# Kernel tuning notes

Measured on AMD Instinct MI355X. Metric: run time of the kernel, lower is better.

Reference implementation:

```python
import jax, jax.numpy as jnp
import numpy as np

K = 256      # embedding size k
STATE = 128  # latent state size
IN = 64      # external input size
OBS = 64     # observation size
L = 512      # sequence length (time-major)
B = 256      # batch size


def _glorot(key, shape):
    return jax.random.normal(key, shape, dtype=jnp.float32) / float(np.sqrt(shape[0]))


def setup_inputs():
    key = jax.random.key(0)
    ks = jax.random.split(key, 12)
    p = {}
    p["external_input_seq"] = jax.random.normal(ks[0], (L, B, IN), dtype=jnp.float32)
    p["observations_seq"] = jax.random.normal(ks[1], (L, B, OBS), dtype=jnp.float32)
    p["eps"] = jax.random.normal(ks[2], (L, B, STATE), dtype=jnp.float32)  # reparam noise
    # PreProcess: Linear + tanh
    p["Wu"] = _glorot(ks[3], (IN, K)); p["bu"] = jnp.zeros((K,), jnp.float32)
    p["Wx"] = _glorot(ks[4], (OBS, K)); p["bx"] = jnp.zeros((K,), jnp.float32)
    # input_rnn: vanilla tanh RNN, 1 layer, k -> k
    p["W_ih"] = _glorot(ks[5], (K, K)); p["b_ih"] = jnp.zeros((K,), jnp.float32)
    p["W_hh"] = _glorot(ks[6], (K, K)); p["b_hh"] = jnp.zeros((K,), jnp.float32)
    # posterior_a_layer: MLP(2k, k, k, 1) = Linear -> tanh -> Linear
    p["Wa1"] = _glorot(ks[7], (2 * K, K)); p["ba1"] = jnp.zeros((K,), jnp.float32)
    p["Wa2"] = _glorot(ks[8], (K, K)); p["ba2"] = jnp.zeros((K,), jnp.float32)

    def dblock_params(k1, in_dim, hid, out):
        kk = jax.random.split(k1, 4)
        return (_glorot(kk[0], (in_dim, hid)), jnp.zeros((hid,), jnp.float32),
                _glorot(kk[1], (in_dim, hid)), jnp.zeros((hid,), jnp.float32),
                _glorot(kk[2], (hid, out)), jnp.zeros((out,), jnp.float32),
                _glorot(kk[3], (hid, out)), jnp.zeros((out,), jnp.float32))

    names = ["f1_W", "f1_b", "f2_W", "f2_b", "mu_W", "mu_b", "ls_W", "ls_b"]
    for pref, kk in (("post_", ks[9]), ("prior_", ks[10])):
        vals = dblock_params(kk, STATE + K, 2 * K, STATE)
        for n, v in zip(names, vals):
            p[pref + n] = v
    return p


def _dblock(x, f1_W, f1_b, f2_W, f2_b, mu_W, mu_b, ls_W, ls_b):
    # TD-VAE DBlock: gated hidden, then mu / logsigma heads
    t = jnp.tanh(x @ f1_W + f1_b) * jax.nn.sigmoid(x @ f2_W + f2_b)
    return t @ mu_W + mu_b, t @ ls_W + ls_b


def reference(external_input_seq, observations_seq, eps, Wu, bu, Wx, bx,
              W_ih, b_ih, W_hh, b_hh, Wa1, ba1, Wa2, ba2,
              post_f1_W, post_f1_b, post_f2_W, post_f2_b, post_mu_W, post_mu_b, post_ls_W, post_ls_b,
              prior_f1_W, prior_f1_b, prior_f2_W, prior_f2_b, prior_mu_W, prior_mu_b, prior_ls_W, prior_ls_b):
    batch = external_input_seq.shape[1]
    u_emb = jnp.tanh(external_input_seq @ Wu + bu)   # [L,B,K]
    x_emb = jnp.tanh(observations_seq @ Wx + bx)     # [L,B,K]

    # input_rnn (tanh RNN) over time, d0 = 0 (memory_state=None)
    def rnn_step(d, x):
        d_new = jnp.tanh(x @ W_ih + b_ih + d @ W_hh + b_hh)
        return d_new, d_new
    d0 = jnp.zeros((batch, W_hh.shape[0]), dtype=u_emb.dtype)
    dn, d_seq = jax.lax.scan(rnn_step, d0, u_emb)    # dn [B,K], d_seq [L,B,K]

    # posterior_a_layer: pointwise MLP; flip(0) then flip(0) is a no-op for a pointwise map
    ad = jnp.concatenate([d_seq, x_emb], axis=-1)    # [L,B,2K]
    a_seq = jnp.tanh(ad @ Wa1 + ba1) @ Wa2 + ba2     # [L,B,K]

    state_size = post_mu_W.shape[1]
    z0 = jnp.zeros((batch, state_size), dtype=u_emb.dtype)

    def step(z_prev, inp):
        a_t, d_t, e_t = inp
        mean_res, logsigma = _dblock(jnp.concatenate([z_prev, a_t], axis=-1),
                                     post_f1_W, post_f1_b, post_f2_W, post_f2_b,
                                     post_mu_W, post_mu_b, post_ls_W, post_ls_b)
        prior_mean = _dblock(jnp.concatenate([z_prev, d_t], axis=-1),
                             prior_f1_W, prior_f1_b, prior_f2_W, prior_f2_b,
                             prior_mu_W, prior_mu_b, prior_ls_W, prior_ls_b)[0]
        mu = prior_mean + mean_res
        # cov = diag(exp(logsigma)) -> std = exp(0.5*logsigma); reparameterized sample
        z_new = mu + jnp.exp(0.5 * logsigma) * e_t
        return z_new, (mu, logsigma)

    zn, (state_mu, state_logsigma) = jax.lax.scan(step, z0, (a_seq, d_seq, eps))
    return state_mu, state_logsigma, dn, zn
```

## Files before the change

### kernel.cpp

```cpp
#include <hip/hip_runtime.h>

#define LSEQ 512
#define BATCH 256
#define KDIM 256
#define STATE 128

using f32x4  = __attribute__((ext_vector_type(4))) float;
using short8 = __attribute__((ext_vector_type(8))) short;
using u32x2  = __attribute__((ext_vector_type(2))) unsigned int;
using u32x4  = __attribute__((ext_vector_type(4))) unsigned int;

__device__ __forceinline__ float bf2f(unsigned short u){
  return __uint_as_float(((unsigned int)u) << 16);
}
__device__ __forceinline__ unsigned short f2bf(float f){
  unsigned int u = __float_as_uint(f);
  u += 0x7FFFu + ((u >> 16) & 1u);
  return (unsigned short)(u >> 16);
}
__device__ __forceinline__ float fast_tanh(float x){
  float ax = fabsf(x);
  float e  = __expf(2.0f * ax);
  float t  = 1.0f - 2.0f / (e + 1.0f);
  return copysignf(t, x);
}
__device__ __forceinline__ float fast_sig(float x){
  return 1.0f / (1.0f + __expf(-x));
}
__device__ __forceinline__ f32x4 mfma16(short8 a, short8 b, f32x4 c){
  return __builtin_amdgcn_mfma_f32_16x16x32_bf16(a, b, c, 0, 0, 0);
}

__device__ __forceinline__ int swz128 (int b){ return b ^ ((((b >> 7) & 7) << 4)); }
__device__ __forceinline__ int swz256 (int b){ return b ^ ((((b >> 8) & 7) << 4)); }
__device__ __forceinline__ int swz512 (int b){ return b ^ ((((b >> 9) & 7) << 4)); }

__device__ __forceinline__ void st_b128_ic(void* p, u32x4 v){
  asm volatile("global_store_dwordx4 %0, %1, off sc0 sc1" :: "v"(p), "v"(v) : "memory");
}
__device__ __forceinline__ void st_b64_ic(void* p, u32x2 v){
  asm volatile("global_store_dwordx2 %0, %1, off sc0 sc1" :: "v"(p), "v"(v) : "memory");
}
#define LD2_IC(dst, p) asm volatile("global_load_dwordx2 %0, %1, off sc0 sc1" : "=v"(dst) : "v"(p) : "memory")

__device__ __forceinline__ f32x4 cvt4(u32x2 q){
  f32x4 r;
  r[0] = __uint_as_float(q[0] << 16);
  r[1] = __uint_as_float(q[0] & 0xFFFF0000u);
  r[2] = __uint_as_float(q[1] << 16);
  r[3] = __uint_as_float(q[1] & 0xFFFF0000u);
  return r;
}

struct WDesc { const float* src; unsigned short* dst; int K, N, ld, rowoff, coloff; };
struct WDescs { WDesc d[24]; };

__global__ __launch_bounds__(256,4) void convert_weights(WDescs ds){
  WDesc w = ds.d[blockIdx.y];
  int total = w.K * w.N;
  int idx = blockIdx.x * 256 + threadIdx.x;
  if (idx < total){
    int n = idx / w.K;
    int k = idx - n * w.K;
    w.dst[idx] = f2bf(w.src[(size_t)(w.rowoff + k) * w.ld + w.coloff + n]);
  }
}

__global__ __launch_bounds__(256,1) void init_flags(int* flags){
  flags[blockIdx.x * 256 + threadIdx.x] = 0;
}

__global__ __launch_bounds__(256,4) void compose_GA(
    const float* __restrict__ Wa2, const float* __restrict__ ba2,
    const unsigned short* __restrict__ fAp,
    const float* __restrict__ pf1b, const float* __restrict__ pf2b,
    unsigned short* __restrict__ GA, float* __restrict__ gb)
{
  const int n = blockIdx.x;
  const int k2 = threadIdx.x;
  const unsigned short* fr = fAp + (size_t)n * 256;
  const float* wr = Wa2 + (size_t)k2 * 256;
  float s = 0.f;
  for (int j = 0; j < 256; j++) s += wr[j] * bf2f(fr[j]);
  GA[(size_t)n * 256 + k2] = f2bf(s);
  if (k2 == 0){
    float b = 0.f;
    for (int j = 0; j < 256; j++) b += ba2[j] * bf2f(fr[j]);
    gb[n] = b + ((n < 512) ? pf1b[n] : pf2b[n - 512]);
  }
}

struct GArg {
  const void* A; const unsigned short* Bt; const float* bias; const float* bias2;
  unsigned short* C; int lda, ldc, coff, K, act, a_f32;
};
struct GArg2 {
  const unsigned short* A; const unsigned short* Bt; const float* bias; const float* bias2;
  unsigned short* C; int lda, ldc, coff, K, act;
};

__device__ void gemm_multi_body(const GArg ga, int bx, int by, int tid, char* lsraw){
  char* lsA = lsraw;
  char* lsB = lsraw + 16384;
  const int wave = tid >> 6, lane = tid & 63;
  const int col_l = lane & 15, rgrp = lane >> 4;
  const int m0 = bx * 128, n0 = by * 128;
  const int wm = (wave >> 1) * 64, wn = (wave & 1) * 64;

  f32x4 acc[4][4];
  const f32x4 z4 = {0.f,0.f,0.f,0.f};
  #pragma unroll
  for (int i=0;i<4;i++){ acc[i][0]=z4; acc[i][1]=z4; acc[i][2]=z4; acc[i][3]=z4; }

  const int srow = tid >> 1;
  const int sbe  = (tid & 1) * 32;

  for (int k0 = 0; k0 < ga.K; k0 += 64){
    uint4 av[4], bv[4];
    if (ga.a_f32){
      const float* Ap = (const float*)ga.A + (size_t)(m0 + srow) * ga.lda + k0 + sbe;
      uint4 fv[8];
      #pragma unroll
      for (int i=0;i<8;i++) fv[i] = *(const uint4*)((const char*)Ap + i*16);
      #pragma unroll
      for (int i=0;i<4;i++){
        const float* f = (const float*)&fv[i*2];
        uint4 o;
        o.x = (unsigned)f2bf(f[0]) | ((unsigned)f2bf(f[1]) << 16);
        o.y = (unsigned)f2bf(f[2]) | ((unsigned)f2bf(f[3]) << 16);
        o.z = (unsigned)f2bf(f[4]) | ((unsigned)f2bf(f[5]) << 16);
        o.w = (unsigned)f2bf(f[6]) | ((unsigned)f2bf(f[7]) << 16);
        av[i] = o;
      }
    } else {
      const unsigned short* Ap = (const unsigned short*)ga.A + (size_t)(m0 + srow) * ga.lda + k0 + sbe;
      #pragma unroll
      for (int i=0;i<4;i++) av[i] = *(const uint4*)((const char*)Ap + i*16);
    }
    const unsigned short* Bp = ga.Bt + (size_t)(n0 + srow) * ga.K + k0 + sbe;
    #pragma unroll
    for (int i=0;i<4;i++) bv[i] = *(const uint4*)((const char*)Bp + i*16);

    __syncthreads();
    #pragma unroll
    for (int i=0;i<4;i++){
      *(uint4*)(lsA + swz128(srow*128 + sbe*2 + i*16)) = av[i];
      *(uint4*)(lsB + swz128(srow*128 + sbe*2 + i*16)) = bv[i];
    }
    __syncthreads();
    #pragma unroll
    for (int kk=0; kk<2; kk++){
      short8 af[4], bfr[4];
      #pragma unroll
      for (int mt=0; mt<4; mt++)
        af[mt] = *(const short8*)(lsA + swz128((wm + mt*16 + col_l)*128 + kk*64 + rgrp*16));
      #pragma unroll
      for (int nt=0; nt<4; nt++)
        bfr[nt] = *(const short8*)(lsB + swz128((wn + nt*16 + col_l)*128 + kk*64 + rgrp*16));
      #pragma unroll
      for (int mt=0; mt<4; mt++)
        #pragma unroll
        for (int nt=0; nt<4; nt++)
          acc[mt][nt] = mfma16(af[mt], bfr[nt], acc[mt][nt]);
    }
  }
  #pragma unroll
  for (int nt=0; nt<4; nt++){
    int col = n0 + wn + nt*16 + col_l;
    const float* bsrc = (col < 512) ? ga.bias : ga.bias2;
    float bb = bsrc ? bsrc[col & 511] : 0.0f;
    #pragma unroll
    for (int mt=0; mt<4; mt++){
      #pragma unroll
      for (int r=0; r<4; r++){
        int row = m0 + wm + mt*16 + rgrp*4 + r;
        float v = acc[mt][nt][r] + bb;
        if (ga.act == 1) v = fast_tanh(v);
        ga.C[(size_t)row * ga.ldc + ga.coff + col] = f2bf(v);
      }
    }
  }
}

__device__ void gemm_glds_body(const GArg2 ga, int bx, int by, int tid, char* lsraw){
  const int wave = tid >> 6, lane = tid & 63;
  const int col_l = lane & 15, rgrp = lane >> 4;
  const int m0 = bx * 128, n0 = by * 128;
  const int wm = (wave >> 1) * 64, wn = (wave & 1) * 64;

  const int lrow = lane >> 3;
  const int scol = (((lane & 7) ^ lrow) << 3);

  auto STAGE = [&](int k0, int buf){
    #pragma unroll
    for (int c = 0; c < 4; c++){
      int srow = wave*32 + c*8 + lrow;
      const unsigned short* pa = ga.A  + (size_t)(m0 + srow) * ga.lda + k0 + scol;
      const unsigned short* pb = ga.Bt + (size_t)(n0 + srow) * ga.K  + k0 + scol;
      __builtin_amdgcn_global_load_lds(
          (const __attribute__((address_space(1))) unsigned int*)pa,
          (__attribute__((address_space(3))) unsigned int*)(lsraw + buf*32768 + wave*4096 + c*1024),
          16, 0, 0);
      __builtin_amdgcn_global_load_lds(
          (const __attribute__((address_space(1))) unsigned int*)pb,
          (__attribute__((address_space(3))) unsigned int*)(lsraw + buf*32768 + 16384 + wave*4096 + c*1024),
          16, 0, 0);
    }
  };

  f32x4 acc[4][4];
  const f32x4 z4 = {0.f,0.f,0.f,0.f};
  #pragma unroll
  for (int i=0;i<4;i++){ acc[i][0]=z4; acc[i][1]=z4; acc[i][2]=z4; acc[i][3]=z4; }

  const int niter = ga.K >> 6;
  STAGE(0, 0);

  for (int i = 0; i < niter; i++){
    if (i + 1 < niter){
      STAGE((i+1)*64, (i+1) & 1);
      asm volatile("s_waitcnt vmcnt(8)" ::: "memory");
    } else {
      asm volatile("s_waitcnt vmcnt(0)" ::: "memory");
    }
    __syncthreads();
    const char* la = lsraw + (i&1)*32768;
    const char* lb = la + 16384;
    #pragma unroll
    for (int kk=0; kk<2; kk++){
      short8 af[4], bfr[4];
      #pragma unroll
      for (int mt=0; mt<4; mt++)
        af[mt] = *(const short8*)(la + swz128((wm + mt*16 + col_l)*128 + kk*64 + rgrp*16));
      #pragma unroll
      for (int nt=0; nt<4; nt++)
        bfr[nt] = *(const short8*)(lb + swz128((wn + nt*16 + col_l)*128 + kk*64 + rgrp*16));
      #pragma unroll
      for (int mt=0; mt<4; mt++)
        #pragma unroll
        for (int nt=0; nt<4; nt++)
          acc[mt][nt] = mfma16(af[mt], bfr[nt], acc[mt][nt]);
    }
    __syncthreads();
  }

  #pragma unroll
  for (int nt=0; nt<4; nt++){
    int col = n0 + wn + nt*16 + col_l;
    const float* bsrc = (col < 512) ? ga.bias : ga.bias2;
    float bb = bsrc ? bsrc[col & 511] : 0.0f;
    #pragma unroll
    for (int mt=0; mt<4; mt++){
      #pragma unroll
      for (int r=0; r<4; r++){
        int row = m0 + wm + mt*16 + rgrp*4 + r;
        float v = acc[mt][nt][r] + bb;
        if (ga.act == 1) v = fast_tanh(v);
        ga.C[(size_t)row * ga.ldc + ga.coff + col] = f2bf(v);
      }
    }
  }
}

__device__ void rnn_body(
    const unsigned short* rnn_in, const unsigned short* Whh_t, const float* b_hh,
    unsigned short* cat_d, float* dn_out, unsigned short* d_state,
    int t0, int nsteps, int bx, int tid, char* lsraw)
{
  char* dls = lsraw;
  const int wave = tid >> 6, lane = tid & 63;
  const int col_l = lane & 15, rgrp = lane >> 4;
  const int brow0 = bx * 16;
  const int ncol = wave * 64;

  short8 bfr[4][8];
  #pragma unroll
  for (int nt=0; nt<4; nt++){
    const unsigned short* bp = Whh_t + (size_t)(ncol + nt*16 + col_l) * 256;
    #pragma unroll
    for (int kk=0; kk<8; kk++)
      bfr[nt][kk] = *(const short8*)(bp + kk*32 + rgrp*8);
  }
  float bias[4];
  #pragma unroll
  for (int nt=0; nt<4; nt++) bias[nt] = b_hh[ncol + nt*16 + col_l];

  if (t0 == 0){
    for (int i = tid; i < 16*256; i += 256){
      int row = i >> 8, col = i & 255;
      *(unsigned short*)(dls + swz512(row*512 + col*2)) = 0;
    }
  } else {
    const unsigned short* ds = d_state + (size_t)brow0 * 256;
    for (int i = tid; i < 16*256; i += 256){
      int row = i >> 8, col = i & 255;
      *(unsigned short*)(dls + swz512(row*512 + col*2)) = ds[row*256 + col];
    }
  }
  __syncthreads();

  for (int tl=0; tl<nsteps; tl++){
    unsigned short rv[4][4];
    const unsigned short* rp = rnn_in + (size_t)(tl*BATCH + brow0) * 256;
    #pragma unroll
    for (int nt=0; nt<4; nt++)
      #pragma unroll
      for (int r=0; r<4; r++)
        rv[nt][r] = rp[(size_t)(rgrp*4 + r)*256 + ncol + nt*16 + col_l];

    f32x4 acc[4];
    const f32x4 z4 = {0.f,0.f,0.f,0.f};
    acc[0]=z4; acc[1]=z4; acc[2]=z4; acc[3]=z4;
    #pragma unroll
    for (int kk=0; kk<8; kk++){
      short8 af = *(const short8*)(dls + swz512((lane & 15)*512 + kk*64 + rgrp*16));
      #pragma unroll
      for (int nt=0; nt<4; nt++)
        acc[nt] = mfma16(af, bfr[nt][kk], acc[nt]);
    }
    __syncthreads();
    #pragma unroll
    for (int nt=0; nt<4; nt++){
      #pragma unroll
      for (int r=0; r<4; r++){
        float h = acc[nt][r] + bf2f(rv[nt][r]) + bias[nt];
        float d = fast_tanh(h);
        int row = rgrp*4 + r, col = ncol + nt*16 + col_l;
        unsigned short db = f2bf(d);
        *(unsigned short*)(dls + swz512(row*512 + col*2)) = db;
        cat_d[(size_t)(tl*BATCH + brow0 + row)*512 + col] = db;
        if (t0 + tl == LSEQ-1) dn_out[(size_t)(brow0 + row)*256 + col] = d;
      }
    }
    __syncthreads();
  }
  unsigned short* dso = d_state + (size_t)brow0 * 256;
  for (int i = tid; i < 16*256; i += 256){
    int row = i >> 8, col = i & 255;
    dso[row*256 + col] = *(const unsigned short*)(dls + swz512(row*512 + col*2));
  }
}

__device__ void zrec_body(
    const unsigned short* preP, const unsigned short* preQ,
    const unsigned short* Wzz, const unsigned short* W2,
    const float* pmub, const float* plsb, const float* qmub,
    const float* eps, float* out_mu, float* out_ls, float* out_zn,
    unsigned short* z_state, unsigned short* mb, int* flags,
    int t0, int nsteps, int poff, int bid, int tid, char* lsraw)
{
  unsigned short* zls = (unsigned short*)lsraw;
  unsigned short* tls = (unsigned short*)(lsraw + 4096);
  unsigned short* bls = (unsigned short*)(lsraw + 12288);
  const int wave = tid >> 6, lane = tid & 63;
  const int col_l = lane & 15, rgrp = lane >> 4;
  const int c   = (bid >> 3) & 3;
  const int g   = (bid & 7) + ((bid >> 5) << 3);
  const int brow0 = g * 16;
  const int NT2 = (c < 2) ? 2 : 1;

  const unsigned short* pre = (c < 2) ? preP : preQ;
  const int cb = (c & 1) * 256;

  short8 w1[2][2][4];
  {
    const unsigned short* wz = Wzz + (size_t)c * 65536;
    #pragma unroll
    for (int m=0; m<2; m++)
      #pragma unroll
      for (int nt=0; nt<2; nt++){
        int n = wave*32 + nt*16 + col_l;
        #pragma unroll
        for (int kk=0; kk<4; kk++)
          w1[m][nt][kk] = *(const short8*)(wz + (size_t)(m*256 + n)*128 + kk*32 + rgrp*8);
      }
  }
  short8 w2r[2][8];
  {
    const unsigned short* wp = W2 + (size_t)c * 65536;
    #pragma unroll
    for (int nt=0; nt<2; nt++){
      if (nt < NT2){
        int ccol = wave*(16*((c<2)?2:1)) + nt*16;
        int mat = (c < 2) ? (ccol >> 7) : 0;
        int n   = (ccol & 127) + col_l;
        #pragma unroll
        for (int kk=0; kk<8; kk++)
          w2r[nt][kk] = *(const short8*)(wp + (size_t)(mat*128 + n)*256 + kk*32 + rgrp*8);
      }
    }
  }
  int* const fline  = flags + g*32;
  int* const myflag = fline + c;

  if (t0 == 0){
    for (int i = tid; i < 16*128; i += 512){
      int row = i >> 7, col = i & 127;
      *(unsigned short*)((char*)zls + swz256(row*256 + col*2)) = 0;
    }
  } else {
    const unsigned short* zs = z_state + (size_t)brow0 * 128;
    for (int i = tid; i < 16*128; i += 512){
      int row = i >> 7, col = i & 127;
      *(unsigned short*)((char*)zls + swz256(row*256 + col*2)) = zs[row*128 + col];
    }
  }
  __syncthreads();

  auto LD_PRE = [&](int tl, unsigned short (&pa_)[2][4], unsigned short (&pb_)[2][4]){
    const unsigned short* bA = pre + ((size_t)(poff + tl)*BATCH + brow0)*1024 + cb;
    #pragma unroll
    for (int nt=0; nt<2; nt++)
      #pragma unroll
      for (int r=0; r<4; r++){
        int row = rgrp*4 + r, col = wave*32 + nt*16 + col_l;
        pa_[nt][r] = bA[(size_t)row*1024 + col];
        pb_[nt][r] = bA[(size_t)row*1024 + 512 + col];
      }
  };

  const int rrow = tid >> 5;
  const int rc0  = (tid & 31) * 4;
  const f32x4 bp4 = *(const f32x4*)(pmub + rc0);
  const f32x4 bl4 = *(const f32x4*)(plsb + rc0);
  const f32x4 bq4 = *(const f32x4*)(qmub + rc0);

  unsigned short pa0[2][4], pb0[2][4], pa1[2][4], pb1[2][4];
  LD_PRE(0, pa0, pb0);

  const f32x4 z4 = {0.f,0.f,0.f,0.f};
  for (int tl=0; tl<nsteps; ++tl){
    size_t growr = (size_t)(t0+tl)*BATCH + brow0 + rrow;
    f32x4 er = *(const f32x4*)(eps + growr*STATE + rc0);
    int nx = (tl+1 < nsteps) ? tl+1 : tl;
    LD_PRE(nx, pa1, pb1);
    const int par = (t0 + tl) & 1;

    short8 af1[4];
    #pragma unroll
    for (int kk=0; kk<4; kk++)
      af1[kk] = *(const short8*)((const char*)zls + swz256((lane & 15)*256 + kk*64 + rgrp*16));
    f32x4 a1[2][2];
    a1[0][0]=z4; a1[0][1]=z4; a1[1][0]=z4; a1[1][1]=z4;
    #pragma unroll
    for (int kk=0; kk<4; kk++)
      #pragma unroll
      for (int m=0; m<2; m++)
        #pragma unroll
        for (int nt=0; nt<2; nt++)
          a1[m][nt] = mfma16(af1[kk], w1[m][nt][kk], a1[m][nt]);

    #pragma unroll
    for (int nt=0; nt<2; nt++)
      #pragma unroll
      for (int r=0; r<4; r++){
        float h1 = a1[0][nt][r] + bf2f(pa0[nt][r]);
        float h2 = a1[1][nt][r] + bf2f(pb0[nt][r]);
        float tv = fast_tanh(h1) * fast_sig(h2);
        int row = rgrp*4 + r, tcol = wave*32 + nt*16 + col_l;
        *(unsigned short*)((char*)tls + swz512(row*512 + tcol*2)) = f2bf(tv);
      }
    __syncthreads();

    f32x4 a2[2];
    a2[0]=z4; a2[1]=z4;
    #pragma unroll
    for (int kk=0; kk<8; kk++){
      short8 af2 = *(const short8*)((const char*)tls + swz512((lane & 15)*512 + kk*64 + rgrp*16));
      #pragma unroll
      for (int nt=0; nt<2; nt++)
        if (nt < NT2) a2[nt] = mfma16(af2, w2r[nt][kk], a2[nt]);
    }
    if (c < 2){
      #pragma unroll
      for (int nt=0; nt<2; nt++)
        #pragma unroll
        for (int r=0; r<4; r++)
          bls[(rgrp*4 + r)*256 + wave*32 + nt*16 + col_l] = f2bf(a2[nt][r]);
    } else {
      #pragma unroll
      for (int r=0; r<4; r++)
        bls[(rgrp*4 + r)*128 + wave*16 + col_l] = f2bf(a2[0][r]);
    }
    __syncthreads();

    unsigned short* slot = mb + (size_t)((g*2 + par)*4 + c)*4096;
    if (c < 2){
      u32x4 v = *(const u32x4*)((const char*)bls + tid*16);
      st_b128_ic(slot + tid*8, v);
    } else {
      u32x2 v = *(const u32x2*)((const char*)bls + tid*8);
      st_b64_ic(slot + tid*4, v);
    }
    asm volatile("s_waitcnt vmcnt(0)" ::: "memory");
    __syncthreads();
    const int target = t0 + tl + 1;
    if (tid == 0)
      __hip_atomic_store(myflag, target, __ATOMIC_RELAXED, __HIP_MEMORY_SCOPE_AGENT);

    if (lane == 0){
      u32x4 F;
      for (;;){
        asm volatile("global_load_dwordx4 %0, %1, off sc0 sc1\n\ts_waitcnt vmcnt(0)"
                     : "=v"(F) : "v"(fline) : "memory");
        int ok = 1;
        #pragma unroll
        for (int p=0; p<4; p++)
          if (p != c && (int)F[p] < target) ok = 0;
        if (ok) break;
        __builtin_amdgcn_s_sleep(1);
      }
    }

    const unsigned short* mbb = mb + (size_t)((g*2 + par)*4)*4096;
    const unsigned short* s0 = mbb;
    const unsigned short* s1 = mbb + 4096;
    const unsigned short* s2 = mbb + 8192;
    const unsigned short* s3 = mbb + 12288;
    u32x2 q0,q1,q2,q3,q4,q5;
    LD2_IC(q0, s0 + rrow*256 + rc0);
    LD2_IC(q1, s1 + rrow*256 + rc0);
    LD2_IC(q2, s0 + rrow*256 + 128 + rc0);
    LD2_IC(q3, s1 + rrow*256 + 128 + rc0);
    LD2_IC(q4, s2 + rrow*128 + rc0);
    LD2_IC(q5, s3 + rrow*128 + rc0);
    asm volatile("s_waitcnt vmcnt(0)" ::: "memory");
    __builtin_amdgcn_sched_barrier(0);

    f32x4 mup = cvt4(q0) + cvt4(q1);
    f32x4 lsv = cvt4(q2) + cvt4(q3) + bl4;
    f32x4 muq = cvt4(q4) + cvt4(q5);
    f32x4 muv = (muq + bq4) + (mup + bp4);
    f32x4 zv;
    #pragma unroll
    for (int i=0; i<4; i++) zv[i] = muv[i] + __expf(0.5f * lsv[i]) * er[i];

    unsigned int lo = (unsigned)f2bf(zv[0]) | ((unsigned)f2bf(zv[1]) << 16);
    unsigned int hi = (unsigned)f2bf(zv[2]) | ((unsigned)f2bf(zv[3]) << 16);
    uint2 zp; zp.x = lo; zp.y = hi;
    *(uint2*)((char*)zls + swz256(rrow*256 + rc0*2)) = zp;
    if (c == 0){
      *(f32x4*)(out_mu + growr*STATE + rc0) = muv;
      *(f32x4*)(out_ls + growr*STATE + rc0) = lsv;
      if (t0 + tl == LSEQ-1)
        *(f32x4*)(out_zn + ((size_t)(brow0 + rrow))*STATE + rc0) = zv;
    }
    __syncthreads();

    #pragma unroll
    for (int nt=0; nt<2; nt++)
      #pragma unroll
      for (int r=0; r<4; r++){ pa0[nt][r] = pa1[nt][r]; pb0[nt][r] = pb1[nt][r]; }
  }

  if (c == 0){
    unsigned short* zso = z_state + (size_t)brow0 * 128;
    for (int i = tid; i < 16*128; i += 512){
      int row = i >> 7, col = i & 127;
      zso[row*128 + col] = *(const unsigned short*)((const char*)zls + swz256(row*256 + col*2));
    }
  }
}

struct MegaArgs {
  const unsigned short *zP, *zQ, *Wzz, *W2;
  const float *pmub, *plsb, *qmub, *eps;
  float *out_mu, *out_ls, *out_zn;
  unsigned short *zst, *mb; int *flags;
  int t0z, nsz, poff;
  int stage, gx;
  GArg  e0, e1;
  GArg2 p0, p1;
  const unsigned short *rnn_in, *Whh; const float* b_hh;
  unsigned short* cat_d; float* dn_out; unsigned short* dstt; int t0r, nsr;
};

__global__ __launch_bounds__(512,1) void mega(MegaArgs A){
  __shared__ __align__(16) char smem[131072];
  const int tid = threadIdx.x;
  if ((int)blockIdx.x < 64){
    if (A.nsz > 0)
      zrec_body(A.zP, A.zQ, A.Wzz, A.W2, A.pmub, A.plsb, A.qmub, A.eps,
                A.out_mu, A.out_ls, A.out_zn, A.zst, A.mb, A.flags,
                A.t0z, A.nsz, A.poff, (int)blockIdx.x, tid, smem);
    return;
  }
  const int pb = (int)blockIdx.x - 64;
  const int half = tid >> 8, ltid = tid & 255;
  char* ls = smem + half*65536;
  const int lg = pb*2 + half;
  if (A.stage == 0){
    int bxx = lg % A.gx, t = lg / A.gx;
    gemm_multi_body((t >= 2) ? A.e1 : A.e0, bxx, t & 1, ltid, ls);
  } else if (A.stage == 1 || A.stage == 3){
    int bxx = lg % A.gx, by = lg / A.gx;
    gemm_glds_body(A.p0, bxx, by, ltid, ls);
  } else if (A.stage == 2){
    rnn_body(A.rnn_in, A.Whh, A.b_hh, A.cat_d, A.dn_out, A.dstt, A.t0r, A.nsr, lg, ltid, ls);
  } else if (A.stage == 4){
    int bxx = lg % A.gx, t = lg / A.gx;
    gemm_glds_body((t >> 3) ? A.p1 : A.p0, bxx, t & 7, ltid, ls);
  }
}

extern "C" void kernel_launch(void* const* d_in, const int* in_sizes, int n_in,
                              void* d_out, int out_size, void* d_ws, size_t ws_size,
                              hipStream_t stream)
{
  const float* ext = (const float*)d_in[0];
  const float* obs = (const float*)d_in[1];
  const float* eps = (const float*)d_in[2];
  const float* Wu  = (const float*)d_in[3];
  const float* bu  = (const float*)d_in[4];
  const float* Wx  = (const float*)d_in[5];
  const float* bx  = (const float*)d_in[6];
  const float* W_ih= (const float*)d_in[7];
  const float* b_ih= (const float*)d_in[8];
  const float* W_hh= (const float*)d_in[9];
  const float* b_hh= (const float*)d_in[10];
  const float* Wa1 = (const float*)d_in[11];
  const float* ba1 = (const float*)d_in[12];
  const float* Wa2 = (const float*)d_in[13];
  const float* ba2 = (const float*)d_in[14];
  const float* pf1W= (const float*)d_in[15]; const float* pf1b = (const float*)d_in[16];
  const float* pf2W= (const float*)d_in[17]; const float* pf2b = (const float*)d_in[18];
  const float* pmuW= (const float*)d_in[19]; const float* pmub = (const float*)d_in[20];
  const float* plsW= (const float*)d_in[21]; const float* plsb = (const float*)d_in[22];
  const float* qf1W= (const float*)d_in[23]; const float* qf1b = (const float*)d_in[24];
  const float* qf2W= (const float*)d_in[25]; const float* qf2b = (const float*)d_in[26];
  const float* qmuW= (const float*)d_in[27]; const float* qmub = (const float*)d_in[28];

  int NC = 0;
  const int cands[5] = {4,8,16,32,64};
  size_t rows = 0;
  for (int ci=0; ci<5; ci++){
    size_t r = (size_t)(LSEQ/cands[ci])*BATCH;
    size_t elems = 2600000 + r*5120;
    if (elems * 2 <= ws_size){ NC = cands[ci]; rows = r; break; }
  }
  if (!NC) return;
  const int nsteps = LSEQ/NC;
  const int gx = (int)(rows/128);

  unsigned short* ws = (unsigned short*)d_ws;
  size_t off = 0;
  auto alloc = [&](size_t elems){
    unsigned short* p = ws + off;
    off += (elems + 127) & ~(size_t)127;
    return p;
  };

  unsigned short* Wu_t  = alloc(64*256);
  unsigned short* Wx_t  = alloc(64*256);
  unsigned short* Wih_t = alloc(256*256);
  unsigned short* Whh_t = alloc(256*256);
  unsigned short* Wa1_t = alloc(512*256);
  unsigned short* fAp   = alloc(1024*256);
  unsigned short* fAq   = alloc(1024*256);
  unsigned short* GAp   = alloc(1024*256);
  float*          gbp   = (float*)alloc(2048);
  unsigned short* Wzz   = alloc(4*2*256*128);
  unsigned short* W2z   = alloc(4*2*128*256);
  unsigned short* d_state = alloc(256*256);
  unsigned short* z_state = alloc(256*128);
  unsigned short* mbx  = alloc(16*2*4*4096);
  int*   flg  = (int*)alloc(4096);
  unsigned short* bufA  = alloc(rows*256);
  unsigned short* bufB  = alloc(rows*256);
  unsigned short* bufC  = alloc(rows*512);
  unsigned short* preP0 = alloc(rows*1024);
  unsigned short* preP1 = alloc(rows*1024);
  unsigned short* preQ0 = alloc(rows*1024);
  unsigned short* preQ1 = alloc(rows*1024);
  if (off * sizeof(unsigned short) > ws_size) return;

  float* out_mu = (float*)d_out;
  float* out_ls = out_mu + (size_t)LSEQ*BATCH*STATE;
  float* out_dn = out_ls + (size_t)LSEQ*BATCH*STATE;
  float* out_zn = out_dn + (size_t)BATCH*KDIM;

  WDescs wd;
  int wi = 0;
  auto add = [&](const float* s, unsigned short* d, int Kk, int Nn, int ld, int ro, int co){
    wd.d[wi].src = s; wd.d[wi].dst = d; wd.d[wi].K = Kk; wd.d[wi].N = Nn;
    wd.d[wi].ld = ld; wd.d[wi].rowoff = ro; wd.d[wi].coloff = co; wi++;
  };
  add(Wu,   Wu_t,  64, 256, 256, 0, 0);
  add(Wx,   Wx_t,  64, 256, 256, 0, 0);
  add(W_ih, Wih_t, 256, 256, 256, 0, 0);
  add(W_hh, Whh_t, 256, 256, 256, 0, 0);
  add(Wa1,  Wa1_t, 512, 256, 256, 0, 0);
  add(pf1W, fAp,            256, 512, 512, 128, 0);
  add(pf2W, fAp + 512*256,  256, 512, 512, 128, 0);
  add(qf1W, fAq,            256, 512, 512, 128, 0);
  add(qf2W, fAq + 512*256,  256, 512, 512, 128, 0);
  for (int c=0; c<4; c++){
    const float* s1 = (c < 2) ? pf1W : qf1W;
    const float* s2 = (c < 2) ? pf2W : qf2W;
    add(s1, Wzz + (size_t)(c*2+0)*32768, 128, 256, 512, 0, (c&1)*256);
    add(s2, Wzz + (size_t)(c*2+1)*32768, 128, 256, 512, 0, (c&1)*256);
  }
  add(pmuW, W2z + (size_t)(0*2+0)*32768, 256, 128, 128, 0,   0);
  add(plsW, W2z + (size_t)(0*2+1)*32768, 256, 128, 128, 0,   0);
  add(pmuW, W2z + (size_t)(1*2+0)*32768, 256, 128, 128, 256, 0);
  add(plsW, W2z + (size_t)(1*2+1)*32768, 256, 128, 128, 256, 0);
  add(qmuW, W2z + (size_t)(2*2+0)*32768, 256, 128, 128, 0,   0);
  add(qmuW, W2z + (size_t)(3*2+0)*32768, 256, 128, 128, 256, 0);

  convert_weights<<<dim3(512, wi), 256, 0, stream>>>(wd);
  compose_GA<<<1024, 256, 0, stream>>>(Wa2, ba2, fAp, pf1b, pf2b, GAp, gbp);
  init_flags<<<8, 256, 0, stream>>>(flg);

  int s4 = (nsteps/5) & ~1;
  int segs[5] = {s4, s4, s4, s4, nsteps - 4*s4};

  auto zfill = [&](MegaArgs& A, int c_z){
    A.zP = (c_z & 1) ? preP1 : preP0;
    A.zQ = (c_z & 1) ? preQ1 : preQ0;
    A.Wzz = Wzz; A.W2 = W2z; A.pmub = pmub; A.plsb = plsb; A.qmub = qmub;
    A.eps = eps; A.out_mu = out_mu; A.out_ls = out_ls; A.out_zn = out_zn;
    A.zst = z_state; A.mb = mbx; A.flags = flg;
  };

  for (int c=0; c<NC; ++c){
    const size_t row0 = (size_t)c * nsteps * BATCH;
    unsigned short* pP = (c & 1) ? preP1 : preP0;
    unsigned short* pQ = (c & 1) ? preQ1 : preQ0;
    int zo = 0;
    for (int st=0; st<5; st++){
      MegaArgs A{};
      zfill(A, c-1);
      A.t0z = (c-1)*nsteps + zo;
      A.poff = zo;
      A.nsz = (c == 0) ? 0 : segs[st];
      zo += segs[st];
      A.stage = st; A.gx = gx;
      int nphys;
      if (st == 0){
        A.e0 = GArg{ext + row0*64, Wu_t, bu, bu, bufA, 64, 256, 0,   64, 1, 1};
        A.e1 = GArg{obs + row0*64, Wx_t, bx, bx, bufC, 64, 512, 256, 64, 1, 1};
        nphys = gx*2;
      } else if (st == 1){
        A.p0 = GArg2{bufA, Wih_t, b_ih, b_ih, bufB, 256, 256, 0, 256, 0};
        nphys = gx;
      } else if (st == 2){
        A.rnn_in = bufB; A.Whh = Whh_t; A.b_hh = b_hh; A.cat_d = bufC;
        A.dn_out = out_dn; A.dstt = d_state; A.t0r = c*nsteps; A.nsr = nsteps;
        nphys = 8;
      } else if (st == 3){
        A.p0 = GArg2{bufC, Wa1_t, ba1, ba1, bufA, 512, 256, 0, 512, 1};
        nphys = gx;
      } else {
        A.p0 = GArg2{bufA, GAp, gbp, gbp + 512, pP, 256, 1024, 0, 256, 0};
        A.p1 = GArg2{bufC, fAq, qf1b, qf2b, pQ, 512, 1024, 0, 256, 0};
        nphys = gx*8;
      }
      mega<<<64 + nphys, 512, 0, stream>>>(A);
    }
  }
  {
    MegaArgs A{};
    zfill(A, NC-1);
    A.t0z = (NC-1)*nsteps; A.poff = 0; A.nsz = nsteps;
    A.stage = 5; A.gx = gx;
    mega<<<64, 512, 0, stream>>>(A);
  }
}
```

Measured before the change: 3.517 ms.

## Halve mega kernel LDS, single-buffer GEMM, stage epilogue through LDS, reweight segments

Shared memory in the mega kernel drops from 128 KB to 64 KB and the launch bounds ask for 4 blocks per CU instead of 1, aiming to co-schedule more blocks. To fit, the global_load_lds GEMM loses its double buffering and now waits for each K tile before computing. Its epilogue now writes the tile to LDS and then does coalesced 16-byte global stores instead of scattered 2-byte stores. The pipeline segments are also split unevenly, with a short head and a long tail. Risks: the tighter launch bounds may cause heavy register spills in the GEMM and RNN bodies, the loads are no longer overlapped with compute, and the recurrence bodies may need more than 64 KB of LDS.

```diff
diff --git a/kernel.cpp b/kernel.cpp
--- a/kernel.cpp
+++ b/kernel.cpp
@@ -191,7 +191,7 @@
   const int lrow = lane >> 3;
   const int scol = (((lane & 7) ^ lrow) << 3);
 
-  auto STAGE = [&](int k0, int buf){
+  auto STAGE = [&](int k0){
     #pragma unroll
     for (int c = 0; c < 4; c++){
       int srow = wave*32 + c*8 + lrow;
@@ -199,11 +199,11 @@
       const unsigned short* pb = ga.Bt + (size_t)(n0 + srow) * ga.K  + k0 + scol;
       __builtin_amdgcn_global_load_lds(
           (const __attribute__((address_space(1))) unsigned int*)pa,
-          (__attribute__((address_space(3))) unsigned int*)(lsraw + buf*32768 + wave*4096 + c*1024),
+          (__attribute__((address_space(3))) unsigned int*)(lsraw + wave*4096 + c*1024),
           16, 0, 0);
       __builtin_amdgcn_global_load_lds(
           (const __attribute__((address_space(1))) unsigned int*)pb,
-          (__attribute__((address_space(3))) unsigned int*)(lsraw + buf*32768 + 16384 + wave*4096 + c*1024),
+          (__attribute__((address_space(3))) unsigned int*)(lsraw + 16384 + wave*4096 + c*1024),
           16, 0, 0);
     }
   };
@@ -214,27 +214,20 @@
   for (int i=0;i<4;i++){ acc[i][0]=z4; acc[i][1]=z4; acc[i][2]=z4; acc[i][3]=z4; }
 
   const int niter = ga.K >> 6;
-  STAGE(0, 0);
 
   for (int i = 0; i < niter; i++){
-    if (i + 1 < niter){
-      STAGE((i+1)*64, (i+1) & 1);
-      asm volatile("s_waitcnt vmcnt(8)" ::: "memory");
-    } else {
-      asm volatile("s_waitcnt vmcnt(0)" ::: "memory");
-    }
-    __syncthreads();
-    const char* la = lsraw + (i&1)*32768;
-    const char* lb = la + 16384;
+    STAGE(i*64);
+    asm volatile("s_waitcnt vmcnt(0)" ::: "memory");
+    __syncthreads();
     #pragma unroll
     for (int kk=0; kk<2; kk++){
       short8 af[4], bfr[4];
       #pragma unroll
       for (int mt=0; mt<4; mt++)
-        af[mt] = *(const short8*)(la + swz128((wm + mt*16 + col_l)*128 + kk*64 + rgrp*16));
+        af[mt] = *(const short8*)(lsraw + swz128((wm + mt*16 + col_l)*128 + kk*64 + rgrp*16));
       #pragma unroll
       for (int nt=0; nt<4; nt++)
-        bfr[nt] = *(const short8*)(lb + swz128((wn + nt*16 + col_l)*128 + kk*64 + rgrp*16));
+        bfr[nt] = *(const short8*)(lsraw + 16384 + swz128((wn + nt*16 + col_l)*128 + kk*64 + rgrp*16));
       #pragma unroll
       for (int mt=0; mt<4; mt++)
         #pragma unroll
@@ -244,21 +237,31 @@
     __syncthreads();
   }
 
+  unsigned short* lt = (unsigned short*)lsraw;
   #pragma unroll
   for (int nt=0; nt<4; nt++){
-    int col = n0 + wn + nt*16 + col_l;
+    int cl = wn + nt*16 + col_l;
+    int col = n0 + cl;
     const float* bsrc = (col < 512) ? ga.bias : ga.bias2;
     float bb = bsrc ? bsrc[col & 511] : 0.0f;
     #pragma unroll
     for (int mt=0; mt<4; mt++){
       #pragma unroll
       for (int r=0; r<4; r++){
-        int row = m0 + wm + mt*16 + rgrp*4 + r;
+        int rl = wm + mt*16 + rgrp*4 + r;
         float v = acc[mt][nt][r] + bb;
         if (ga.act == 1) v = fast_tanh(v);
-        ga.C[(size_t)row * ga.ldc + ga.coff + col] = f2bf(v);
-      }
-    }
+        lt[rl*128 + cl] = f2bf(v);
+      }
+    }
+  }
+  __syncthreads();
+  #pragma unroll
+  for (int i=0; i<8; i++){
+    int idx = i*256 + tid;
+    int row = idx >> 4, ch = idx & 15;
+    u32x4 v = *(const u32x4*)(lt + row*128 + ch*8);
+    *(u32x4*)(ga.C + (size_t)(m0 + row) * ga.ldc + ga.coff + n0 + ch*8) = v;
   }
 }
 
@@ -575,8 +578,8 @@
   unsigned short* cat_d; float* dn_out; unsigned short* dstt; int t0r, nsr;
 };
 
-__global__ __launch_bounds__(512,1) void mega(MegaArgs A){
-  __shared__ __align__(16) char smem[131072];
+__global__ __launch_bounds__(512,4) void mega(MegaArgs A){
+  __shared__ __align__(16) char smem[65536];
   const int tid = threadIdx.x;
   if ((int)blockIdx.x < 64){
     if (A.nsz > 0)
@@ -587,7 +590,7 @@
   }
   const int pb = (int)blockIdx.x - 64;
   const int half = tid >> 8, ltid = tid & 255;
-  char* ls = smem + half*65536;
+  char* ls = smem + half*32768;
   const int lg = pb*2 + half;
   if (A.stage == 0){
     int bxx = lg % A.gx, t = lg / A.gx;
@@ -711,8 +714,14 @@
   compose_GA<<<1024, 256, 0, stream>>>(Wa2, ba2, fAp, pf1b, pf2b, GAp, gbp);
   init_flags<<<8, 256, 0, stream>>>(flg);
 
-  int s4 = (nsteps/5) & ~1;
-  int segs[5] = {s4, s4, s4, s4, nsteps - 4*s4};
+  const int wseg[5] = {12, 12, 12, 26, 66};
+  int segs[5]; int sacc = 0;
+  for (int i=0; i<4; i++){
+    int s = (nsteps * wseg[i] / 128) & ~1;
+    if (s < 2) s = 2;
+    segs[i] = s; sacc += s;
+  }
+  segs[4] = nsteps - sacc;
 
   auto zfill = [&](MegaArgs& A, int c_z){
     A.zP = (c_z & 1) ? preP1 : preP0;
```

New measurement: 9.670 ms. +175.0%, slower.
